# Kernel tuning notes

Hardware: AMD Instinct MI355X
Metric: run time of the kernel (lower is better)

Reference implementation:

```python
import jax, jax.numpy as jnp
import numpy as np

H = 10        # hidden size hardcoded in the torch module
MAX_PAD = 3   # static upper bound on zero_pad values (setup generates 0..2)
EPS = 1e-5    # torch BatchNorm1d default eps


def _batchnorm(x, gamma, beta):
    # training-mode BatchNorm1d: batch mean, biased batch variance
    m = jnp.mean(x, axis=0)
    v = jnp.var(x, axis=0)
    return (x - m) * jax.lax.rsqrt(v + EPS) * gamma + beta


def setup_inputs() -> dict:
    N, D = 65536, 512
    key = jax.random.key(0)
    ks = jax.random.split(key, 12)
    return {
        "x": jax.random.normal(ks[0], (N, D), jnp.float32),
        "zero_pad": jax.random.randint(ks[1], (N,), 0, MAX_PAD),
        "broad_id": jnp.sort(jax.random.randint(ks[2], (N,), 0, 8192)),
        "W1": jax.random.normal(ks[3], (H, D), jnp.float32) * 0.05,
        "b1": jax.random.normal(ks[4], (H,), jnp.float32) * 0.05,
        "g1": jnp.ones((H,), jnp.float32),
        "be1": jnp.zeros((H,), jnp.float32),
        "W_ih": jax.random.normal(ks[5], (4 * H, H), jnp.float32) * 0.2,
        "W_hh": jax.random.normal(ks[6], (4 * H, H), jnp.float32) * 0.2,
        "b_ih": jax.random.normal(ks[7], (4 * H,), jnp.float32) * 0.2,
        "b_hh": jax.random.normal(ks[8], (4 * H,), jnp.float32) * 0.2,
        "g2": jnp.ones((H,), jnp.float32),
        "be2": jnp.zeros((H,), jnp.float32),
        "W2": jax.random.normal(ks[9], (1, H), jnp.float32) * 0.3,
        "b2": jnp.zeros((1,), jnp.float32),
    }


def reference(x, zero_pad, broad_id, W1, b1, g1, be1, W_ih, W_hh, b_ih, b_hh, g2, be2, W2, b2):
    x1 = _batchnorm(x @ W1.T + b1, g1, be1)  # [N, H]
    # group boundary: last step of each broad_id run (incl. the final step)
    bnd = jnp.concatenate([broad_id[1:] != broad_id[:-1], jnp.array([True])])

    def cell(xin, h, c):
        g = xin @ W_ih.T + b_ih + h @ W_hh.T + b_hh  # [4H]
        i, f, gg, o = jnp.split(g, 4)                # torch gate order i,f,g,o
        i = jax.nn.sigmoid(i); f = jax.nn.sigmoid(f)
        gg = jnp.tanh(gg);     o = jax.nn.sigmoid(o)
        c2 = f * c + i * gg
        return o * jnp.tanh(c2), c2

    zin = jnp.zeros((H,), x1.dtype)

    def step(carry, inp):
        h, c, sh, sc, cnt = carry
        xi, zp, b = inp
        # dynamic zero-pad repeats, expressed as fixed-length masked loop
        for k in range(MAX_PAD):
            h2, c2 = cell(zin, h, c)
            m = k < zp
            h = jnp.where(m, h2, h)
            c = jnp.where(m, c2, c)
        ht, ct = cell(xi, h, c)
        # NOTE: within a group, (h, c) is NOT advanced by ht/ct -- faithful to source
        sh = sh + ht; sc = sc + ct; cnt = cnt + 1.0
        hn = jnp.where(b, sh / cnt, h)
        cn = jnp.where(b, sc / cnt, c)
        sh = jnp.where(b, 0.0, sh)
        sc = jnp.where(b, 0.0, sc)
        cnt = jnp.where(b, 0.0, cnt)
        return (hn, cn, sh, sc, cnt), ht

    z = jnp.zeros((H,), x1.dtype)
    init = (z, z, z, z, jnp.float32(0.0))
    _, outs = jax.lax.scan(step, init, (x1, zero_pad, bnd))  # outs: [N, H]
    out = _batchnorm(outs, g2, be2) @ W2.T + b2              # [N, 1]
    return jnp.tanh(out)
```

## Files before the change

kernel.cpp:

```cpp
#include <hip/hip_runtime.h>

#define NR 65536
#define DIN 512
#define H 10
#define G4 40
#define EPSB 1e-5f
#define CHUNK 32
#define WPB 4
#define WARM 32
#define SPW (WARM + CHUNK)
#define SLOTS (WARM + WPB*CHUNK)
#define NBLK (NR / (WPB * CHUNK))

__device__ __forceinline__ float fast_rcp(float x) {
  return __builtin_amdgcn_rcpf(x);
}
__device__ __forceinline__ float rlane(float v, int l) {
  return __int_as_float(__builtin_amdgcn_readlane(__float_as_int(v), l));
}
#define QP(v, code)                                                       \
  __int_as_float(__builtin_amdgcn_mov_dpp(__float_as_int(v), (code), 0xF, \
                                          0xF, true))
#define ROR(v, N)                                                          \
  __int_as_float(__builtin_amdgcn_mov_dpp(__float_as_int(v), 0x120 + (N), \
                                          0xF, 0xF, true))

#define LOG2E 1.442695041f

__global__ __launch_bounds__(256) void k1_proj(const float* __restrict__ x,
                                               const float* __restrict__ W1,
                                               const float* __restrict__ b1,
                                               float* __restrict__ y,
                                               float* __restrict__ part1) {
  const int tid = threadIdx.x;
  const int lane = tid & 63;
  const int wv = tid >> 6;
  const int gw = blockIdx.x * 4 + wv;

  float w[H][8];
#pragma unroll
  for (int j = 0; j < H; ++j) {
    float4 a = *(const float4*)&W1[j * DIN + lane * 8];
    float4 b = *(const float4*)&W1[j * DIN + lane * 8 + 4];
    w[j][0] = a.x; w[j][1] = a.y; w[j][2] = a.z; w[j][3] = a.w;
    w[j][4] = b.x; w[j][5] = b.y; w[j][6] = b.z; w[j][7] = b.w;
  }
  const float bj = (lane < H) ? b1[lane] : 0.0f;
  float s1 = 0.0f, s2 = 0.0f;

  const int r0 = gw * 32;
  float4 xa = *(const float4*)&x[(size_t)r0 * DIN + lane * 8];
  float4 xb = *(const float4*)&x[(size_t)r0 * DIN + lane * 8 + 4];

  for (int i = 0; i < 32; ++i) {
    const int r = r0 + i;
    const int rn = (i + 1 < 32) ? r + 1 : r;
    float4 na = *(const float4*)&x[(size_t)rn * DIN + lane * 8];
    float4 nb = *(const float4*)&x[(size_t)rn * DIN + lane * 8 + 4];

    float acc[H];
#pragma unroll
    for (int j = 0; j < H; ++j) {
      float s = xa.x * w[j][0];
      s = fmaf(xa.y, w[j][1], s);
      s = fmaf(xa.z, w[j][2], s);
      s = fmaf(xa.w, w[j][3], s);
      s = fmaf(xb.x, w[j][4], s);
      s = fmaf(xb.y, w[j][5], s);
      s = fmaf(xb.z, w[j][6], s);
      s = fmaf(xb.w, w[j][7], s);
      acc[j] = s;
    }
#pragma unroll
    for (int j = 0; j < H; ++j) {
      float a = acc[j];
      a += ROR(a, 1);
      a += ROR(a, 2);
      a += ROR(a, 4);
      a += ROR(a, 8);
      acc[j] = a;
    }
    float tot[H];
#pragma unroll
    for (int j = 0; j < H; ++j) {
      float p0 = rlane(acc[j], 0);
      float p1 = rlane(acc[j], 16);
      float p2 = rlane(acc[j], 32);
      float p3 = rlane(acc[j], 48);
      tot[j] = (p0 + p1) + (p2 + p3);
    }
    float v = tot[0];
#pragma unroll
    for (int j = 1; j < H; ++j) v = (lane == j) ? tot[j] : v;
    if (lane < H) {
      v += bj;
      y[(size_t)r * H + lane] = v;
      s1 += v;
      s2 += v * v;
    }
    xa = na; xb = nb;
  }

  __shared__ float red[4][2 * H];
  if (lane < H) { red[wv][lane] = s1; red[wv][H + lane] = s2; }
  __syncthreads();
  if (tid < 2 * H) {
    float s = red[0][tid] + red[1][tid] + red[2][tid] + red[3][tid];
    part1[tid * NBLK + blockIdx.x] = s;
  }
}

__global__ __launch_bounds__(256) void k1b_red(const float* __restrict__ part1,
                                               const float* __restrict__ g1,
                                               const float* __restrict__ be1,
                                               float* __restrict__ ab1) {
  __shared__ float tot[2 * H];
  const int tid = threadIdx.x;
  const int lane = tid & 63;
  const int wv = tid >> 6;
  for (int j = wv; j < 2 * H; j += 4) {
    float s = 0.0f;
    for (int b = lane; b < NBLK; b += 64) s += part1[j * NBLK + b];
    s += ROR(s, 1); s += ROR(s, 2); s += ROR(s, 4); s += ROR(s, 8);
    float p0 = rlane(s, 0), p1 = rlane(s, 16);
    float p2 = rlane(s, 32), p3 = rlane(s, 48);
    if (lane == 0) tot[j] = (p0 + p1) + (p2 + p3);
  }
  __syncthreads();
  if (tid < H) {
    float m = tot[tid] * (1.0f / NR);
    float v = tot[H + tid] * (1.0f / NR) - m * m;
    float inv = rsqrtf(v + EPSB);
    ab1[tid] = inv * g1[tid];
    ab1[H + tid] = be1[tid] - m * inv * g1[tid];
  }
}

__global__ __launch_bounds__(256) void k2_xg(const float* __restrict__ y,
                                             const float* __restrict__ ab1,
                                             const float* __restrict__ Wih,
                                             float* __restrict__ xg) {
  __shared__ float wl[G4 * H];
  __shared__ float A[H], B[H];
  const int tid = threadIdx.x;
  for (int i = tid; i < G4 * H; i += 256) wl[i] = Wih[i];
  if (tid < H) {
    A[tid] = ab1[tid];
    B[tid] = ab1[H + tid];
  }
  __syncthreads();

  const int t = blockIdx.x * 256 + tid;
  float x1[H];
#pragma unroll
  for (int m = 0; m < H; ++m) x1[m] = fmaf(y[(size_t)t * H + m], A[m], B[m]);

  float out[G4];
#pragma unroll
  for (int g = 0; g < 4; ++g) {
#pragma unroll
    for (int k = 0; k < H; ++k) {
      const int j = g * H + k;
      float s = 0.0f;
#pragma unroll
      for (int m = 0; m < H; ++m) s = fmaf(wl[j * H + m], x1[m], s);
      out[k * 4 + g] = s;
    }
  }
  float4* o4 = (float4*)(xg + (size_t)t * G4);
#pragma unroll
  for (int q = 0; q < G4 / 4; ++q) o4[q] = ((const float4*)out)[q];
}

__device__ __forceinline__ void cell40(float xin, float h, float c,
                                       const float (&w)[H], float bias,
                                       float As2, float Am, float Aa,
                                       float& ht, float& ct) {
  float a0 = bias + xin, a1 = 0.0f;
#pragma unroll
  for (int m = 0; m < H; m += 2) {
    float hm0 = rlane(h, 4 * m);
    float hm1 = rlane(h, 4 * (m + 1));
    a0 = fmaf(w[m], hm0, a0);
    a1 = fmaf(w[m + 1], hm1, a1);
  }
  float a = a0 + a1;
  float e = __builtin_amdgcn_exp2f(a * As2);
  float r = fast_rcp(1.0f + e);
  float gt = fmaf(r, Am, Aa);
  float gi = QP(gt, 0x00);
  float gf = QP(gt, 0x55);
  float gg = QP(gt, 0xAA);
  float go = QP(gt, 0xFF);
  ct = fmaf(gf, c, gi * gg);
  float e2 = __builtin_amdgcn_exp2f(ct * (-2.0f * LOG2E));
  float r2 = fast_rcp(1.0f + e2);
  float th = fmaf(r2, 2.0f, -1.0f);
  ht = go * th;
}

__global__ __launch_bounds__(256) void k3_scan(const float* __restrict__ xg,
                                               const int* __restrict__ zp_arr,
                                               const int* __restrict__ broad,
                                               const float* __restrict__ Whh,
                                               const float* __restrict__ bih,
                                               const float* __restrict__ bhh,
                                               float* __restrict__ outs,
                                               float* __restrict__ part2) {
  __shared__ __align__(16) float sxg[SLOTS * G4 + 64];
  __shared__ int szb[SLOTS];
  __shared__ float red[WPB][2 * H];

  const int tid = threadIdx.x;
  const int blk = blockIdx.x;
  const int tw = blk * (WPB * CHUNK) - WARM;

  {
    const int n4 = SLOTS * (G4 / 4);
    for (int i = tid; i < n4; i += 256) {
      const int slot = i / (G4 / 4);
      const int q = i - slot * (G4 / 4);
      int t = tw + slot;
      t = t < 0 ? 0 : t;
      ((float4*)sxg)[i] = ((const float4*)&xg[(size_t)t * G4])[q];
    }
    for (int i = tid; i < SLOTS; i += 256) {
      const int t = tw + i;
      const int tc = t < 0 ? 0 : t;
      const int z = zp_arr[tc];
      const int bn = (t + 1 >= NR) ? 1 : ((broad[tc + 1] != broad[tc]) ? 1 : 0);
      szb[i] = z | (bn << 8);
    }
  }
  __syncthreads();

  const int lane = tid & 63;
  const int wv = tid >> 6;

  if (lane < G4) {
    const int u = lane >> 2;
    const int g = lane & 3;

    const int row = g * H + u;
    float w[H];
#pragma unroll
    for (int m = 0; m < H; ++m) w[m] = Whh[row * H + m];
    const float bias = bih[row] + bhh[row];
    const bool isT = (g == 2);
    const float As2 = isT ? (-2.0f * LOG2E) : (-1.0f * LOG2E);
    const float Am = isT ? 2.0f : 1.0f;
    const float Aa = isT ? -1.0f : 0.0f;

    float h = 0.0f, c = 0.0f;
    float sh = 0.0f, sc = 0.0f, cntf = 0.0f;
    float s1 = 0.0f, s2 = 0.0f;

    const int slot0 = wv * CHUNK;
    float xv = sxg[slot0 * G4 + lane];
    int zb = szb[slot0];

    for (int s = 0; s < SPW; ++s) {
      const int slot = slot0 + s;
      const int slotn = (s + 1 < SPW) ? slot + 1 : slot;
      float xn = sxg[slotn * G4 + lane];
      int zbn = szb[slotn];

      const int t = tw + slot;
      if (t >= 0) {
        const int zbu = __builtin_amdgcn_readfirstlane(zb);
        const int zp = zbu & 0xFF;
        for (int p = 0; p < zp; ++p) {
          float h2, c2;
          cell40(0.0f, h, c, w, bias, As2, Am, Aa, h2, c2);
          h = h2; c = c2;
        }
        float ht, ct;
        cell40(xv, h, c, w, bias, As2, Am, Aa, ht, ct);
        sh += ht; sc += ct; cntf += 1.0f;

        if (s >= WARM) {
          if (g == 0) outs[(size_t)t * H + u] = ht;
          s1 += ht;
          s2 += ht * ht;
        }
        if (zbu & 256) {
          const float r = fast_rcp(cntf);
          h = sh * r; c = sc * r;
          sh = 0.0f; sc = 0.0f; cntf = 0.0f;
        }
      }
      xv = xn;
      zb = zbn;
    }
    if (g == 0) {
      red[wv][u] = s1;
      red[wv][H + u] = s2;
    }
  }
  __syncthreads();
  if (tid < 2 * H) {
    float s = red[0][tid] + red[1][tid] + red[2][tid] + red[3][tid];
    part2[tid * NBLK + blk] = s;
  }
}

__global__ __launch_bounds__(256) void k4_red(const float* __restrict__ part2,
                                              const float* __restrict__ g2,
                                              const float* __restrict__ be2,
                                              const float* __restrict__ W2,
                                              const float* __restrict__ b2,
                                              float* __restrict__ cb) {
  __shared__ float tot[2 * H];
  __shared__ float contrib[H];
  const int tid = threadIdx.x;
  const int lane = tid & 63;
  const int wv = tid >> 6;
  for (int j = wv; j < 2 * H; j += 4) {
    float s = 0.0f;
    for (int b = lane; b < NBLK; b += 64) s += part2[j * NBLK + b];
    s += ROR(s, 1); s += ROR(s, 2); s += ROR(s, 4); s += ROR(s, 8);
    float p0 = rlane(s, 0), p1 = rlane(s, 16);
    float p2 = rlane(s, 32), p3 = rlane(s, 48);
    if (lane == 0) tot[j] = (p0 + p1) + (p2 + p3);
  }
  __syncthreads();
  if (tid < H) {
    float m = tot[tid] * (1.0f / NR);
    float v = tot[H + tid] * (1.0f / NR) - m * m;
    float inv = rsqrtf(v + EPSB);
    cb[tid] = inv * g2[tid] * W2[tid];
    contrib[tid] = (be2[tid] - m * inv * g2[tid]) * W2[tid];
  }
  __syncthreads();
  if (tid == 0) {
    float bacc = b2[0];
#pragma unroll
    for (int j = 0; j < H; ++j) bacc += contrib[j];
    cb[H] = bacc;
  }
}

__global__ __launch_bounds__(256) void k5_out(const float* __restrict__ outs,
                                              const float* __restrict__ cb,
                                              float* __restrict__ out) {
  __shared__ float a2s[H];
  __shared__ float b2s;
  const int tid = threadIdx.x;
  if (tid < H) a2s[tid] = cb[tid];
  if (tid == H) b2s = cb[H];
  __syncthreads();
  const int t = blockIdx.x * 256 + tid;
  float s = b2s;
  const float* r = outs + (size_t)t * H;
#pragma unroll
  for (int j = 0; j < H; ++j) s = fmaf(r[j], a2s[j], s);
  out[t] =
      1.0f - 2.0f * fast_rcp(__builtin_amdgcn_exp2f(2.0f * LOG2E * s) + 1.0f);
}

extern "C" void kernel_launch(void* const* d_in, const int* in_sizes, int n_in,
                              void* d_out, int out_size, void* d_ws,
                              size_t ws_size, hipStream_t stream) {
  const float* x = (const float*)d_in[0];
  const int* zp = (const int*)d_in[1];
  const int* broad = (const int*)d_in[2];
  const float* W1 = (const float*)d_in[3];
  const float* b1 = (const float*)d_in[4];
  const float* g1 = (const float*)d_in[5];
  const float* be1 = (const float*)d_in[6];
  const float* Wih = (const float*)d_in[7];
  const float* Whh = (const float*)d_in[8];
  const float* bih = (const float*)d_in[9];
  const float* bhh = (const float*)d_in[10];
  const float* g2 = (const float*)d_in[11];
  const float* be2 = (const float*)d_in[12];
  const float* W2 = (const float*)d_in[13];
  const float* b2 = (const float*)d_in[14];
  float* out = (float*)d_out;

  float* ws = (float*)d_ws;
  float* ab1 = ws;
  float* cb = ws + 32;
  float* part1 = ws + 64;
  float* part2 = part1 + 2 * H * NBLK;
  float* y = part2 + 2 * H * NBLK;
  float* xg = y + (size_t)NR * H;
  float* outs = y;

  k1_proj<<<dim3(512), dim3(256), 0, stream>>>(x, W1, b1, y, part1);
  k1b_red<<<dim3(1), dim3(256), 0, stream>>>(part1, g1, be1, ab1);
  k2_xg<<<dim3(NR / 256), dim3(256), 0, stream>>>(y, ab1, Wih, xg);
  k3_scan<<<dim3(NBLK), dim3(256), 0, stream>>>(xg, zp, broad, Whh, bih, bhh,
                                                outs, part2);
  k4_red<<<dim3(1), dim3(256), 0, stream>>>(part2, g2, be2, W2, b2, cb);
  k5_out<<<dim3(NR / 256), dim3(256), 0, stream>>>(outs, cb, out);
  (void)in_sizes; (void)n_in; (void)out_size; (void)ws_size;
}
```

Before: 282.2 us.

## Fuse all six stages into one cooperative kernel with grid syncs

Replaces the six separate launches (projection, BN1 reduction, gate precompute, scan, BN2 reduction, output) with one cooperative kernel of 512 blocks that uses grid.sync between phases. The projection output y and the scan outputs stay in shared memory, so their global round trips disappear. The intent is to remove launch overhead and DRAM traffic for intermediates. The risks are grid-sync cost, the co-residency requirement (launch_bounds 256,2 with larger LDS use), and lower occupancy in the projection phase.

```diff
diff --git a/kernel.cpp b/kernel.cpp
--- a/kernel.cpp
+++ b/kernel.cpp
@@ -1,4 +1,7 @@
 #include <hip/hip_runtime.h>
+#include <hip/hip_cooperative_groups.h>
+
+namespace cg = cooperative_groups;
 
 #define NR 65536
 #define DIN 512
@@ -9,8 +12,10 @@
 #define WPB 4
 #define WARM 32
 #define SPW (WARM + CHUNK)
-#define SLOTS (WARM + WPB*CHUNK)
-#define NBLK (NR / (WPB * CHUNK))
+#define SLOTS (WARM + WPB * CHUNK)
+#define NBLK 512
+#define RPB (WPB * CHUNK)
+#define LOG2E 1.442695041f
 
 __device__ __forceinline__ float fast_rcp(float x) {
   return __builtin_amdgcn_rcpf(x);
@@ -24,153 +29,6 @@
 #define ROR(v, N)                                                          \
   __int_as_float(__builtin_amdgcn_mov_dpp(__float_as_int(v), 0x120 + (N), \
                                           0xF, 0xF, true))
-
-#define LOG2E 1.442695041f
-
-__global__ __launch_bounds__(256) void k1_proj(const float* __restrict__ x,
-                                               const float* __restrict__ W1,
-                                               const float* __restrict__ b1,
-                                               float* __restrict__ y,
-                                               float* __restrict__ part1) {
-  const int tid = threadIdx.x;
-  const int lane = tid & 63;
-  const int wv = tid >> 6;
-  const int gw = blockIdx.x * 4 + wv;
-
-  float w[H][8];
-#pragma unroll
-  for (int j = 0; j < H; ++j) {
-    float4 a = *(const float4*)&W1[j * DIN + lane * 8];
-    float4 b = *(const float4*)&W1[j * DIN + lane * 8 + 4];
-    w[j][0] = a.x; w[j][1] = a.y; w[j][2] = a.z; w[j][3] = a.w;
-    w[j][4] = b.x; w[j][5] = b.y; w[j][6] = b.z; w[j][7] = b.w;
-  }
-  const float bj = (lane < H) ? b1[lane] : 0.0f;
-  float s1 = 0.0f, s2 = 0.0f;
-
-  const int r0 = gw * 32;
-  float4 xa = *(const float4*)&x[(size_t)r0 * DIN + lane * 8];
-  float4 xb = *(const float4*)&x[(size_t)r0 * DIN + lane * 8 + 4];
-
-  for (int i = 0; i < 32; ++i) {
-    const int r = r0 + i;
-    const int rn = (i + 1 < 32) ? r + 1 : r;
-    float4 na = *(const float4*)&x[(size_t)rn * DIN + lane * 8];
-    float4 nb = *(const float4*)&x[(size_t)rn * DIN + lane * 8 + 4];
-
-    float acc[H];
-#pragma unroll
-    for (int j = 0; j < H; ++j) {
-      float s = xa.x * w[j][0];
-      s = fmaf(xa.y, w[j][1], s);
-      s = fmaf(xa.z, w[j][2], s);
-      s = fmaf(xa.w, w[j][3], s);
-      s = fmaf(xb.x, w[j][4], s);
-      s = fmaf(xb.y, w[j][5], s);
-      s = fmaf(xb.z, w[j][6], s);
-      s = fmaf(xb.w, w[j][7], s);
-      acc[j] = s;
-    }
-#pragma unroll
-    for (int j = 0; j < H; ++j) {
-      float a = acc[j];
-      a += ROR(a, 1);
-      a += ROR(a, 2);
-      a += ROR(a, 4);
-      a += ROR(a, 8);
-      acc[j] = a;
-    }
-    float tot[H];
-#pragma unroll
-    for (int j = 0; j < H; ++j) {
-      float p0 = rlane(acc[j], 0);
-      float p1 = rlane(acc[j], 16);
-      float p2 = rlane(acc[j], 32);
-      float p3 = rlane(acc[j], 48);
-      tot[j] = (p0 + p1) + (p2 + p3);
-    }
-    float v = tot[0];
-#pragma unroll
-    for (int j = 1; j < H; ++j) v = (lane == j) ? tot[j] : v;
-    if (lane < H) {
-      v += bj;
-      y[(size_t)r * H + lane] = v;
-      s1 += v;
-      s2 += v * v;
-    }
-    xa = na; xb = nb;
-  }
-
-  __shared__ float red[4][2 * H];
-  if (lane < H) { red[wv][lane] = s1; red[wv][H + lane] = s2; }
-  __syncthreads();
-  if (tid < 2 * H) {
-    float s = red[0][tid] + red[1][tid] + red[2][tid] + red[3][tid];
-    part1[tid * NBLK + blockIdx.x] = s;
-  }
-}
-
-__global__ __launch_bounds__(256) void k1b_red(const float* __restrict__ part1,
-                                               const float* __restrict__ g1,
-                                               const float* __restrict__ be1,
-                                               float* __restrict__ ab1) {
-  __shared__ float tot[2 * H];
-  const int tid = threadIdx.x;
-  const int lane = tid & 63;
-  const int wv = tid >> 6;
-  for (int j = wv; j < 2 * H; j += 4) {
-    float s = 0.0f;
-    for (int b = lane; b < NBLK; b += 64) s += part1[j * NBLK + b];
-    s += ROR(s, 1); s += ROR(s, 2); s += ROR(s, 4); s += ROR(s, 8);
-    float p0 = rlane(s, 0), p1 = rlane(s, 16);
-    float p2 = rlane(s, 32), p3 = rlane(s, 48);
-    if (lane == 0) tot[j] = (p0 + p1) + (p2 + p3);
-  }
-  __syncthreads();
-  if (tid < H) {
-    float m = tot[tid] * (1.0f / NR);
-    float v = tot[H + tid] * (1.0f / NR) - m * m;
-    float inv = rsqrtf(v + EPSB);
-    ab1[tid] = inv * g1[tid];
-    ab1[H + tid] = be1[tid] - m * inv * g1[tid];
-  }
-}
-
-__global__ __launch_bounds__(256) void k2_xg(const float* __restrict__ y,
-                                             const float* __restrict__ ab1,
-                                             const float* __restrict__ Wih,
-                                             float* __restrict__ xg) {
-  __shared__ float wl[G4 * H];
-  __shared__ float A[H], B[H];
-  const int tid = threadIdx.x;
-  for (int i = tid; i < G4 * H; i += 256) wl[i] = Wih[i];
-  if (tid < H) {
-    A[tid] = ab1[tid];
-    B[tid] = ab1[H + tid];
-  }
-  __syncthreads();
-
-  const int t = blockIdx.x * 256 + tid;
-  float x1[H];
-#pragma unroll
-  for (int m = 0; m < H; ++m) x1[m] = fmaf(y[(size_t)t * H + m], A[m], B[m]);
-
-  float out[G4];
-#pragma unroll
-  for (int g = 0; g < 4; ++g) {
-#pragma unroll
-    for (int k = 0; k < H; ++k) {
-      const int j = g * H + k;
-      float s = 0.0f;
-#pragma unroll
-      for (int m = 0; m < H; ++m) s = fmaf(wl[j * H + m], x1[m], s);
-      out[k * 4 + g] = s;
-    }
-  }
-  float4* o4 = (float4*)(xg + (size_t)t * G4);
-#pragma unroll
-  for (int q = 0; q < G4 / 4; ++q) o4[q] = ((const float4*)out)[q];
-}
 
 __device__ __forceinline__ void cell40(float xin, float h, float c,
                                        const float (&w)[H], float bias,
@@ -199,23 +57,157 @@
   ht = go * th;
 }
 
-__global__ __launch_bounds__(256) void k3_scan(const float* __restrict__ xg,
-                                               const int* __restrict__ zp_arr,
-                                               const int* __restrict__ broad,
-                                               const float* __restrict__ Whh,
-                                               const float* __restrict__ bih,
-                                               const float* __restrict__ bhh,
-                                               float* __restrict__ outs,
-                                               float* __restrict__ part2) {
+__global__ __launch_bounds__(256, 2) void fused_all(
+    const float* __restrict__ x, const int* __restrict__ zp_arr,
+    const int* __restrict__ broad, const float* __restrict__ W1,
+    const float* __restrict__ b1, const float* __restrict__ g1,
+    const float* __restrict__ be1, const float* __restrict__ Wih,
+    const float* __restrict__ Whh, const float* __restrict__ bih,
+    const float* __restrict__ bhh, const float* __restrict__ g2,
+    const float* __restrict__ be2, const float* __restrict__ W2,
+    const float* __restrict__ b2, float* __restrict__ out,
+    float* __restrict__ part1, float* __restrict__ part2,
+    float* __restrict__ xg) {
+  cg::grid_group grid = cg::this_grid();
+
   __shared__ __align__(16) float sxg[SLOTS * G4 + 64];
   __shared__ int szb[SLOTS];
+  __shared__ float y_s[RPB * H];
+  __shared__ float outs_s[RPB * H];
+  __shared__ float wl[G4 * H];
+  __shared__ float AB[2 * H];
   __shared__ float red[WPB][2 * H];
+  __shared__ float tot[2 * H];
+  __shared__ float cbs[H + 2];
 
   const int tid = threadIdx.x;
   const int blk = blockIdx.x;
-  const int tw = blk * (WPB * CHUNK) - WARM;
+  const int lane = tid & 63;
+  const int wv = tid >> 6;
 
   {
+    float w[H][8];
+#pragma unroll
+    for (int j = 0; j < H; ++j) {
+      float4 a = *(const float4*)&W1[j * DIN + lane * 8];
+      float4 b = *(const float4*)&W1[j * DIN + lane * 8 + 4];
+      w[j][0] = a.x; w[j][1] = a.y; w[j][2] = a.z; w[j][3] = a.w;
+      w[j][4] = b.x; w[j][5] = b.y; w[j][6] = b.z; w[j][7] = b.w;
+    }
+    const float bj = (lane < H) ? b1[lane] : 0.0f;
+    float s1 = 0.0f, s2 = 0.0f;
+
+    const int r0 = blk * RPB + wv * 32;
+    float4 xa = *(const float4*)&x[(size_t)r0 * DIN + lane * 8];
+    float4 xb = *(const float4*)&x[(size_t)r0 * DIN + lane * 8 + 4];
+
+    for (int i = 0; i < 32; ++i) {
+      const int r = r0 + i;
+      const int rn = (i + 1 < 32) ? r + 1 : r;
+      float4 na = *(const float4*)&x[(size_t)rn * DIN + lane * 8];
+      float4 nb = *(const float4*)&x[(size_t)rn * DIN + lane * 8 + 4];
+
+      float acc[H];
+#pragma unroll
+      for (int j = 0; j < H; ++j) {
+        float s = xa.x * w[j][0];
+        s = fmaf(xa.y, w[j][1], s);
+        s = fmaf(xa.z, w[j][2], s);
+        s = fmaf(xa.w, w[j][3], s);
+        s = fmaf(xb.x, w[j][4], s);
+        s = fmaf(xb.y, w[j][5], s);
+        s = fmaf(xb.z, w[j][6], s);
+        s = fmaf(xb.w, w[j][7], s);
+        acc[j] = s;
+      }
+#pragma unroll
+      for (int j = 0; j < H; ++j) {
+        float a = acc[j];
+        a += ROR(a, 1);
+        a += ROR(a, 2);
+        a += ROR(a, 4);
+        a += ROR(a, 8);
+        acc[j] = a;
+      }
+      float totj[H];
+#pragma unroll
+      for (int j = 0; j < H; ++j) {
+        float p0 = rlane(acc[j], 0);
+        float p1 = rlane(acc[j], 16);
+        float p2 = rlane(acc[j], 32);
+        float p3 = rlane(acc[j], 48);
+        totj[j] = (p0 + p1) + (p2 + p3);
+      }
+      float v = totj[0];
+#pragma unroll
+      for (int j = 1; j < H; ++j) v = (lane == j) ? totj[j] : v;
+      if (lane < H) {
+        v += bj;
+        y_s[(wv * 32 + i) * H + lane] = v;
+        s1 += v;
+        s2 += v * v;
+      }
+      xa = na; xb = nb;
+    }
+
+    if (lane < H) { red[wv][lane] = s1; red[wv][H + lane] = s2; }
+    __syncthreads();
+    if (tid < 2 * H) {
+      float s = red[0][tid] + red[1][tid] + red[2][tid] + red[3][tid];
+      part1[tid * NBLK + blk] = s;
+    }
+  }
+  __threadfence();
+  grid.sync();
+  __threadfence();
+
+  {
+    for (int j = wv; j < 2 * H; j += 4) {
+      float s = 0.0f;
+      for (int b = lane; b < NBLK; b += 64) s += part1[j * NBLK + b];
+      s += ROR(s, 1); s += ROR(s, 2); s += ROR(s, 4); s += ROR(s, 8);
+      float p0 = rlane(s, 0), p1 = rlane(s, 16);
+      float p2 = rlane(s, 32), p3 = rlane(s, 48);
+      if (lane == 0) tot[j] = (p0 + p1) + (p2 + p3);
+    }
+    for (int i = tid; i < G4 * H; i += 256) wl[i] = Wih[i];
+    __syncthreads();
+    if (tid < H) {
+      float m = tot[tid] * (1.0f / NR);
+      float v = tot[H + tid] * (1.0f / NR) - m * m;
+      float inv = rsqrtf(v + EPSB);
+      AB[tid] = inv * g1[tid];
+      AB[H + tid] = be1[tid] - m * inv * g1[tid];
+    }
+    __syncthreads();
+    if (tid < RPB) {
+      float x1[H];
+#pragma unroll
+      for (int m = 0; m < H; ++m)
+        x1[m] = fmaf(y_s[tid * H + m], AB[m], AB[H + m]);
+      float o[G4];
+#pragma unroll
+      for (int g = 0; g < 4; ++g) {
+#pragma unroll
+        for (int k = 0; k < H; ++k) {
+          const int j = g * H + k;
+          float s = 0.0f;
+#pragma unroll
+          for (int m = 0; m < H; ++m) s = fmaf(wl[j * H + m], x1[m], s);
+          o[k * 4 + g] = s;
+        }
+      }
+      float4* o4 = (float4*)(xg + (size_t)(blk * RPB + tid) * G4);
+#pragma unroll
+      for (int q = 0; q < G4 / 4; ++q) o4[q] = ((const float4*)o)[q];
+    }
+  }
+  __threadfence();
+  grid.sync();
+  __threadfence();
+
+  {
+    const int tw = blk * RPB - WARM;
     const int n4 = SLOTS * (G4 / 4);
     for (int i = tid; i < n4; i += 256) {
       const int slot = i / (G4 / 4);
@@ -231,131 +223,111 @@
       const int bn = (t + 1 >= NR) ? 1 : ((broad[tc + 1] != broad[tc]) ? 1 : 0);
       szb[i] = z | (bn << 8);
     }
-  }
-  __syncthreads();
-
-  const int lane = tid & 63;
-  const int wv = tid >> 6;
-
-  if (lane < G4) {
-    const int u = lane >> 2;
-    const int g = lane & 3;
-
-    const int row = g * H + u;
-    float w[H];
-#pragma unroll
-    for (int m = 0; m < H; ++m) w[m] = Whh[row * H + m];
-    const float bias = bih[row] + bhh[row];
-    const bool isT = (g == 2);
-    const float As2 = isT ? (-2.0f * LOG2E) : (-1.0f * LOG2E);
-    const float Am = isT ? 2.0f : 1.0f;
-    const float Aa = isT ? -1.0f : 0.0f;
-
-    float h = 0.0f, c = 0.0f;
-    float sh = 0.0f, sc = 0.0f, cntf = 0.0f;
-    float s1 = 0.0f, s2 = 0.0f;
-
-    const int slot0 = wv * CHUNK;
-    float xv = sxg[slot0 * G4 + lane];
-    int zb = szb[slot0];
-
-    for (int s = 0; s < SPW; ++s) {
-      const int slot = slot0 + s;
-      const int slotn = (s + 1 < SPW) ? slot + 1 : slot;
-      float xn = sxg[slotn * G4 + lane];
-      int zbn = szb[slotn];
-
-      const int t = tw + slot;
-      if (t >= 0) {
-        const int zbu = __builtin_amdgcn_readfirstlane(zb);
-        const int zp = zbu & 0xFF;
-        for (int p = 0; p < zp; ++p) {
-          float h2, c2;
-          cell40(0.0f, h, c, w, bias, As2, Am, Aa, h2, c2);
-          h = h2; c = c2;
+    __syncthreads();
+
+    if (lane < G4) {
+      const int u = lane >> 2;
+      const int g = lane & 3;
+
+      const int row = g * H + u;
+      float w[H];
+#pragma unroll
+      for (int m = 0; m < H; ++m) w[m] = Whh[row * H + m];
+      const float bias = bih[row] + bhh[row];
+      const bool isT = (g == 2);
+      const float As2 = isT ? (-2.0f * LOG2E) : (-1.0f * LOG2E);
+      const float Am = isT ? 2.0f : 1.0f;
+      const float Aa = isT ? -1.0f : 0.0f;
+
+      float h = 0.0f, c = 0.0f;
+      float sh = 0.0f, sc = 0.0f, cntf = 0.0f;
+      float s1 = 0.0f, s2 = 0.0f;
+
+      const int slot0 = wv * CHUNK;
+      float xv = sxg[slot0 * G4 + lane];
+      int zb = szb[slot0];
+
+      for (int s = 0; s < SPW; ++s) {
+        const int slot = slot0 + s;
+        const int slotn = (s + 1 < SPW) ? slot + 1 : slot;
+        float xn = sxg[slotn * G4 + lane];
+        int zbn = szb[slotn];
+
+        const int t = tw + slot;
+        if (t >= 0) {
+          const int zbu = __builtin_amdgcn_readfirstlane(zb);
+          const int zp = zbu & 0xFF;
+          for (int p = 0; p < zp; ++p) {
+            float h2, c2;
+            cell40(0.0f, h, c, w, bias, As2, Am, Aa, h2, c2);
+            h = h2; c = c2;
+          }
+          float ht, ct;
+          cell40(xv, h, c, w, bias, As2, Am, Aa, ht, ct);
+          sh += ht; sc += ct; cntf += 1.0f;
+
+          if (s >= WARM) {
+            if (g == 0) outs_s[(slot - WARM) * H + u] = ht;
+            s1 += ht;
+            s2 += ht * ht;
+          }
+          if (zbu & 256) {
+            const float r = fast_rcp(cntf);
+            h = sh * r; c = sc * r;
+            sh = 0.0f; sc = 0.0f; cntf = 0.0f;
+          }
         }
-        float ht, ct;
-        cell40(xv, h, c, w, bias, As2, Am, Aa, ht, ct);
-        sh += ht; sc += ct; cntf += 1.0f;
-
-        if (s >= WARM) {
-          if (g == 0) outs[(size_t)t * H + u] = ht;
-          s1 += ht;
-          s2 += ht * ht;
-        }
-        if (zbu & 256) {
-          const float r = fast_rcp(cntf);
-          h = sh * r; c = sc * r;
-          sh = 0.0f; sc = 0.0f; cntf = 0.0f;
-        }
-      }
-      xv = xn;
-      zb = zbn;
-    }
-    if (g == 0) {
-      red[wv][u] = s1;
-      red[wv][H + u] = s2;
-    }
-  }
-  __syncthreads();
-  if (tid < 2 * H) {
-    float s = red[0][tid] + red[1][tid] + red[2][tid] + red[3][tid];
-    part2[tid * NBLK + blk] = s;
-  }
-}
-
-__global__ __launch_bounds__(256) void k4_red(const float* __restrict__ part2,
-                                              const float* __restrict__ g2,
-                                              const float* __restrict__ be2,
-                                              const float* __restrict__ W2,
-                                              const float* __restrict__ b2,
-                                              float* __restrict__ cb) {
-  __shared__ float tot[2 * H];
-  __shared__ float contrib[H];
-  const int tid = threadIdx.x;
-  const int lane = tid & 63;
-  const int wv = tid >> 6;
-  for (int j = wv; j < 2 * H; j += 4) {
-    float s = 0.0f;
-    for (int b = lane; b < NBLK; b += 64) s += part2[j * NBLK + b];
-    s += ROR(s, 1); s += ROR(s, 2); s += ROR(s, 4); s += ROR(s, 8);
-    float p0 = rlane(s, 0), p1 = rlane(s, 16);
-    float p2 = rlane(s, 32), p3 = rlane(s, 48);
-    if (lane == 0) tot[j] = (p0 + p1) + (p2 + p3);
-  }
-  __syncthreads();
-  if (tid < H) {
-    float m = tot[tid] * (1.0f / NR);
-    float v = tot[H + tid] * (1.0f / NR) - m * m;
-    float inv = rsqrtf(v + EPSB);
-    cb[tid] = inv * g2[tid] * W2[tid];
-    contrib[tid] = (be2[tid] - m * inv * g2[tid]) * W2[tid];
-  }
-  __syncthreads();
-  if (tid == 0) {
-    float bacc = b2[0];
-#pragma unroll
-    for (int j = 0; j < H; ++j) bacc += contrib[j];
-    cb[H] = bacc;
-  }
-}
-
-__global__ __launch_bounds__(256) void k5_out(const float* __restrict__ outs,
-                                              const float* __restrict__ cb,
-                                              float* __restrict__ out) {
-  __shared__ float a2s[H];
-  __shared__ float b2s;
-  const int tid = threadIdx.x;
-  if (tid < H) a2s[tid] = cb[tid];
-  if (tid == H) b2s = cb[H];
-  __syncthreads();
-  const int t = blockIdx.x * 256 + tid;
-  float s = b2s;
-  const float* r = outs + (size_t)t * H;
-#pragma unroll
-  for (int j = 0; j < H; ++j) s = fmaf(r[j], a2s[j], s);
-  out[t] =
-      1.0f - 2.0f * fast_rcp(__builtin_amdgcn_exp2f(2.0f * LOG2E * s) + 1.0f);
+        xv = xn;
+        zb = zbn;
+      }
+      if (g == 0) {
+        red[wv][u] = s1;
+        red[wv][H + u] = s2;
+      }
+    }
+    __syncthreads();
+    if (tid < 2 * H) {
+      float s = red[0][tid] + red[1][tid] + red[2][tid] + red[3][tid];
+      part2[tid * NBLK + blk] = s;
+    }
+  }
+  __threadfence();
+  grid.sync();
+  __threadfence();
+
+  {
+    for (int j = wv; j < 2 * H; j += 4) {
+      float s = 0.0f;
+      for (int b = lane; b < NBLK; b += 64) s += part2[j * NBLK + b];
+      s += ROR(s, 1); s += ROR(s, 2); s += ROR(s, 4); s += ROR(s, 8);
+      float p0 = rlane(s, 0), p1 = rlane(s, 16);
+      float p2 = rlane(s, 32), p3 = rlane(s, 48);
+      if (lane == 0) tot[j] = (p0 + p1) + (p2 + p3);
+    }
+    __syncthreads();
+    if (tid < H) {
+      float m = tot[tid] * (1.0f / NR);
+      float v = tot[H + tid] * (1.0f / NR) - m * m;
+      float inv = rsqrtf(v + EPSB);
+      cbs[tid] = inv * g2[tid] * W2[tid];
+      AB[tid] = (be2[tid] - m * inv * g2[tid]) * W2[tid];
+    }
+    __syncthreads();
+    if (tid == 0) {
+      float bacc = b2[0];
+#pragma unroll
+      for (int j = 0; j < H; ++j) bacc += AB[j];
+      cbs[H] = bacc;
+    }
+    __syncthreads();
+    if (tid < RPB) {
+      float s = cbs[H];
+#pragma unroll
+      for (int j = 0; j < H; ++j) s = fmaf(outs_s[tid * H + j], cbs[j], s);
+      out[blk * RPB + tid] =
+          1.0f - 2.0f * fast_rcp(__builtin_amdgcn_exp2f(2.0f * LOG2E * s) + 1.0f);
+    }
+  }
 }
 
 extern "C" void kernel_launch(void* const* d_in, const int* in_sizes, int n_in,
@@ -379,20 +351,16 @@
   float* out = (float*)d_out;
 
   float* ws = (float*)d_ws;
-  float* ab1 = ws;
-  float* cb = ws + 32;
-  float* part1 = ws + 64;
-  float* part2 = part1 + 2 * H * NBLK;
-  float* y = part2 + 2 * H * NBLK;
-  float* xg = y + (size_t)NR * H;
-  float* outs = y;
-
-  k1_proj<<<dim3(512), dim3(256), 0, stream>>>(x, W1, b1, y, part1);
-  k1b_red<<<dim3(1), dim3(256), 0, stream>>>(part1, g1, be1, ab1);
-  k2_xg<<<dim3(NR / 256), dim3(256), 0, stream>>>(y, ab1, Wih, xg);
-  k3_scan<<<dim3(NBLK), dim3(256), 0, stream>>>(xg, zp, broad, Whh, bih, bhh,
-                                                outs, part2);
-  k4_red<<<dim3(1), dim3(256), 0, stream>>>(part2, g2, be2, W2, b2, cb);
-  k5_out<<<dim3(NR / 256), dim3(256), 0, stream>>>(outs, cb, out);
+  float* part1 = ws;
+  float* part2 = ws + 2 * H * NBLK;
+  float* xg = ws + 4 * H * NBLK;
+
+  void* args[] = {(void*)&x,   (void*)&zp,  (void*)&broad, (void*)&W1,
+                  (void*)&b1,  (void*)&g1,  (void*)&be1,   (void*)&Wih,
+                  (void*)&Whh, (void*)&bih, (void*)&bhh,   (void*)&g2,
+                  (void*)&be2, (void*)&W2,  (void*)&b2,    (void*)&out,
+                  (void*)&part1, (void*)&part2, (void*)&xg};
+  hipLaunchCooperativeKernel((const void*)fused_all, dim3(NBLK), dim3(256),
+                             args, 0, stream);
   (void)in_sizes; (void)n_in; (void)out_size; (void)ws_size;
 }
```

Result: slower. 688.6 us (+144.0%).

## Fuse BN1 reduction and input-gate projection into scan; fold BN2 reduction into output kernel

Applied to the files above, without the earlier changes.

The BN1 statistics reduction and the W_ih projection (previously two separate kernels writing a 40-wide xg buffer to global memory) now happen inside the scan kernel. Each block redundantly reduces part1, loads its y slice into shared memory and computes the gate pre-activations locally. Likewise, the BN2 reduction kernel is merged into the output kernel, with every block redoing the small part2 reduction. This removes three launches and the xg global round trip. In exchange, work is duplicated per block and the scan kernel uses more shared memory, which may lower occupancy.

```diff
diff --git a/kernel.cpp b/kernel.cpp
--- a/kernel.cpp
+++ b/kernel.cpp
@@ -11,6 +11,8 @@
 #define SPW (WARM + CHUNK)
 #define SLOTS (WARM + WPB*CHUNK)
 #define NBLK (NR / (WPB * CHUNK))
+#define RPB (WPB * CHUNK)
+#define LOG2E 1.442695041f
 
 __device__ __forceinline__ float fast_rcp(float x) {
   return __builtin_amdgcn_rcpf(x);
@@ -24,8 +26,6 @@
 #define ROR(v, N)                                                          \
   __int_as_float(__builtin_amdgcn_mov_dpp(__float_as_int(v), 0x120 + (N), \
                                           0xF, 0xF, true))
-
-#define LOG2E 1.442695041f
 
 __global__ __launch_bounds__(256) void k1_proj(const float* __restrict__ x,
                                                const float* __restrict__ W1,
@@ -108,68 +108,6 @@
     float s = red[0][tid] + red[1][tid] + red[2][tid] + red[3][tid];
     part1[tid * NBLK + blockIdx.x] = s;
   }
-}
-
-__global__ __launch_bounds__(256) void k1b_red(const float* __restrict__ part1,
-                                               const float* __restrict__ g1,
-                                               const float* __restrict__ be1,
-                                               float* __restrict__ ab1) {
-  __shared__ float tot[2 * H];
-  const int tid = threadIdx.x;
-  const int lane = tid & 63;
-  const int wv = tid >> 6;
-  for (int j = wv; j < 2 * H; j += 4) {
-    float s = 0.0f;
-    for (int b = lane; b < NBLK; b += 64) s += part1[j * NBLK + b];
-    s += ROR(s, 1); s += ROR(s, 2); s += ROR(s, 4); s += ROR(s, 8);
-    float p0 = rlane(s, 0), p1 = rlane(s, 16);
-    float p2 = rlane(s, 32), p3 = rlane(s, 48);
-    if (lane == 0) tot[j] = (p0 + p1) + (p2 + p3);
-  }
-  __syncthreads();
-  if (tid < H) {
-    float m = tot[tid] * (1.0f / NR);
-    float v = tot[H + tid] * (1.0f / NR) - m * m;
-    float inv = rsqrtf(v + EPSB);
-    ab1[tid] = inv * g1[tid];
-    ab1[H + tid] = be1[tid] - m * inv * g1[tid];
-  }
-}
-
-__global__ __launch_bounds__(256) void k2_xg(const float* __restrict__ y,
-                                             const float* __restrict__ ab1,
-                                             const float* __restrict__ Wih,
-                                             float* __restrict__ xg) {
-  __shared__ float wl[G4 * H];
-  __shared__ float A[H], B[H];
-  const int tid = threadIdx.x;
-  for (int i = tid; i < G4 * H; i += 256) wl[i] = Wih[i];
-  if (tid < H) {
-    A[tid] = ab1[tid];
-    B[tid] = ab1[H + tid];
-  }
-  __syncthreads();
-
-  const int t = blockIdx.x * 256 + tid;
-  float x1[H];
-#pragma unroll
-  for (int m = 0; m < H; ++m) x1[m] = fmaf(y[(size_t)t * H + m], A[m], B[m]);
-
-  float out[G4];
-#pragma unroll
-  for (int g = 0; g < 4; ++g) {
-#pragma unroll
-    for (int k = 0; k < H; ++k) {
-      const int j = g * H + k;
-      float s = 0.0f;
-#pragma unroll
-      for (int m = 0; m < H; ++m) s = fmaf(wl[j * H + m], x1[m], s);
-      out[k * 4 + g] = s;
-    }
-  }
-  float4* o4 = (float4*)(xg + (size_t)t * G4);
-#pragma unroll
-  for (int q = 0; q < G4 / 4; ++q) o4[q] = ((const float4*)out)[q];
 }
 
 __device__ __forceinline__ void cell40(float xin, float h, float c,
@@ -199,43 +137,82 @@
   ht = go * th;
 }
 
-__global__ __launch_bounds__(256) void k3_scan(const float* __restrict__ xg,
-                                               const int* __restrict__ zp_arr,
-                                               const int* __restrict__ broad,
-                                               const float* __restrict__ Whh,
-                                               const float* __restrict__ bih,
-                                               const float* __restrict__ bhh,
-                                               float* __restrict__ outs,
-                                               float* __restrict__ part2) {
+__global__ __launch_bounds__(256) void k3_scan(
+    const float* __restrict__ y, const float* __restrict__ part1,
+    const float* __restrict__ g1, const float* __restrict__ be1,
+    const int* __restrict__ zp_arr, const int* __restrict__ broad,
+    const float* __restrict__ Wih, const float* __restrict__ Whh,
+    const float* __restrict__ bih, const float* __restrict__ bhh,
+    float* __restrict__ outs, float* __restrict__ part2) {
   __shared__ __align__(16) float sxg[SLOTS * G4 + 64];
   __shared__ int szb[SLOTS];
+  __shared__ float sy[SLOTS * H];
+  __shared__ float wl[G4 * H];
+  __shared__ float AB[2 * H];
+  __shared__ float tot[2 * H];
   __shared__ float red[WPB][2 * H];
 
   const int tid = threadIdx.x;
   const int blk = blockIdx.x;
-  const int tw = blk * (WPB * CHUNK) - WARM;
-
-  {
-    const int n4 = SLOTS * (G4 / 4);
-    for (int i = tid; i < n4; i += 256) {
-      const int slot = i / (G4 / 4);
-      const int q = i - slot * (G4 / 4);
-      int t = tw + slot;
-      t = t < 0 ? 0 : t;
-      ((float4*)sxg)[i] = ((const float4*)&xg[(size_t)t * G4])[q];
-    }
-    for (int i = tid; i < SLOTS; i += 256) {
-      const int t = tw + i;
-      const int tc = t < 0 ? 0 : t;
-      const int z = zp_arr[tc];
-      const int bn = (t + 1 >= NR) ? 1 : ((broad[tc + 1] != broad[tc]) ? 1 : 0);
-      szb[i] = z | (bn << 8);
-    }
-  }
-  __syncthreads();
-
   const int lane = tid & 63;
   const int wv = tid >> 6;
+  const int tw = blk * RPB - WARM;
+
+  for (int j = wv; j < 2 * H; j += 4) {
+    float s = 0.0f;
+    for (int b = lane; b < NBLK; b += 64) s += part1[j * NBLK + b];
+    s += ROR(s, 1); s += ROR(s, 2); s += ROR(s, 4); s += ROR(s, 8);
+    float p0 = rlane(s, 0), p1 = rlane(s, 16);
+    float p2 = rlane(s, 32), p3 = rlane(s, 48);
+    if (lane == 0) tot[j] = (p0 + p1) + (p2 + p3);
+  }
+  for (int i = tid; i < SLOTS * H; i += 256) {
+    const int slot = i / H;
+    int t = tw + slot;
+    t = t < 0 ? 0 : t;
+    sy[i] = y[(size_t)t * H + (i - slot * H)];
+  }
+  for (int i = tid; i < G4 * H; i += 256) wl[i] = Wih[i];
+  for (int i = tid; i < SLOTS; i += 256) {
+    const int t = tw + i;
+    const int tc = t < 0 ? 0 : t;
+    const int z = zp_arr[tc];
+    const int bn = (t + 1 >= NR) ? 1 : ((broad[tc + 1] != broad[tc]) ? 1 : 0);
+    szb[i] = z | (bn << 8);
+  }
+  __syncthreads();
+
+  if (tid < H) {
+    float m = tot[tid] * (1.0f / NR);
+    float v = tot[H + tid] * (1.0f / NR) - m * m;
+    float inv = rsqrtf(v + EPSB);
+    AB[tid] = inv * g1[tid];
+    AB[H + tid] = be1[tid] - m * inv * g1[tid];
+  }
+  __syncthreads();
+
+  if (tid < SLOTS) {
+    float x1[H];
+#pragma unroll
+    for (int m = 0; m < H; ++m)
+      x1[m] = fmaf(sy[tid * H + m], AB[m], AB[H + m]);
+    float o[G4];
+#pragma unroll
+    for (int g = 0; g < 4; ++g) {
+#pragma unroll
+      for (int k = 0; k < H; ++k) {
+        const int j = g * H + k;
+        float s = 0.0f;
+#pragma unroll
+        for (int m = 0; m < H; ++m) s = fmaf(wl[j * H + m], x1[m], s);
+        o[k * 4 + g] = s;
+      }
+    }
+    float4* o4 = (float4*)&sxg[tid * G4];
+#pragma unroll
+    for (int q = 0; q < G4 / 4; ++q) o4[q] = ((const float4*)o)[q];
+  }
+  __syncthreads();
 
   if (lane < G4) {
     const int u = lane >> 2;
@@ -304,14 +281,16 @@
   }
 }
 
-__global__ __launch_bounds__(256) void k4_red(const float* __restrict__ part2,
+__global__ __launch_bounds__(256) void k5_out(const float* __restrict__ part2,
                                               const float* __restrict__ g2,
                                               const float* __restrict__ be2,
                                               const float* __restrict__ W2,
                                               const float* __restrict__ b2,
-                                              float* __restrict__ cb) {
+                                              const float* __restrict__ outs,
+                                              float* __restrict__ out) {
   __shared__ float tot[2 * H];
   __shared__ float contrib[H];
+  __shared__ float cbs[H + 1];
   const int tid = threadIdx.x;
   const int lane = tid & 63;
   const int wv = tid >> 6;
@@ -328,7 +307,7 @@
     float m = tot[tid] * (1.0f / NR);
     float v = tot[H + tid] * (1.0f / NR) - m * m;
     float inv = rsqrtf(v + EPSB);
-    cb[tid] = inv * g2[tid] * W2[tid];
+    cbs[tid] = inv * g2[tid] * W2[tid];
     contrib[tid] = (be2[tid] - m * inv * g2[tid]) * W2[tid];
   }
   __syncthreads();
@@ -336,24 +315,14 @@
     float bacc = b2[0];
 #pragma unroll
     for (int j = 0; j < H; ++j) bacc += contrib[j];
-    cb[H] = bacc;
-  }
-}
-
-__global__ __launch_bounds__(256) void k5_out(const float* __restrict__ outs,
-                                              const float* __restrict__ cb,
-                                              float* __restrict__ out) {
-  __shared__ float a2s[H];
-  __shared__ float b2s;
-  const int tid = threadIdx.x;
-  if (tid < H) a2s[tid] = cb[tid];
-  if (tid == H) b2s = cb[H];
+    cbs[H] = bacc;
+  }
   __syncthreads();
   const int t = blockIdx.x * 256 + tid;
-  float s = b2s;
+  float s = cbs[H];
   const float* r = outs + (size_t)t * H;
 #pragma unroll
-  for (int j = 0; j < H; ++j) s = fmaf(r[j], a2s[j], s);
+  for (int j = 0; j < H; ++j) s = fmaf(r[j], cbs[j], s);
   out[t] =
       1.0f - 2.0f * fast_rcp(__builtin_amdgcn_exp2f(2.0f * LOG2E * s) + 1.0f);
 }
@@ -379,20 +348,16 @@
   float* out = (float*)d_out;
 
   float* ws = (float*)d_ws;
-  float* ab1 = ws;
-  float* cb = ws + 32;
-  float* part1 = ws + 64;
-  float* part2 = part1 + 2 * H * NBLK;
-  float* y = part2 + 2 * H * NBLK;
-  float* xg = y + (size_t)NR * H;
-  float* outs = y;
+  float* part1 = ws;
+  float* part2 = ws + 2 * H * NBLK;
+  float* y = ws + 4 * H * NBLK;
+  float* outs = y + (size_t)NR * H;
 
   k1_proj<<<dim3(512), dim3(256), 0, stream>>>(x, W1, b1, y, part1);
-  k1b_red<<<dim3(1), dim3(256), 0, stream>>>(part1, g1, be1, ab1);
-  k2_xg<<<dim3(NR / 256), dim3(256), 0, stream>>>(y, ab1, Wih, xg);
-  k3_scan<<<dim3(NBLK), dim3(256), 0, stream>>>(xg, zp, broad, Whh, bih, bhh,
-                                                outs, part2);
-  k4_red<<<dim3(1), dim3(256), 0, stream>>>(part2, g2, be2, W2, b2, cb);
-  k5_out<<<dim3(NR / 256), dim3(256), 0, stream>>>(outs, cb, out);
+  k3_scan<<<dim3(NBLK), dim3(256), 0, stream>>>(y, part1, g1, be1, zp, broad,
+                                                Wih, Whh, bih, bhh, outs,
+                                                part2);
+  k5_out<<<dim3(NR / 256), dim3(256), 0, stream>>>(part2, g2, be2, W2, b2,
+                                                   outs, out);
   (void)in_sizes; (void)n_in; (void)out_size; (void)ws_size;
 }
```

After: 274.1 us (median of 2 runs). -2.9%, faster.
